# Optimization experiments

Measured on AMD Instinct MI355X. Metric: run time of the kernel, lower is better.

Reference implementation:

```python
import jax, jax.numpy as jnp
import numpy as np

IN_FEATURES = 1024
OUT_FEATURES = 1024
NUM_GRIDS = 8
GRID_MIN, GRID_MAX = -2.0, 2.0
DENOM = (GRID_MAX - GRID_MIN) / (NUM_GRIDS - 1)
LN_EPS = 1e-5
GRID = jnp.linspace(GRID_MIN, GRID_MAX, NUM_GRIDS)


def setup_inputs() -> dict:
    key = jax.random.key(0)
    k_x, k_sw, k_bw = jax.random.split(key, 3)
    N = 8192
    x = jax.random.normal(k_x, (N, IN_FEATURES), dtype=jnp.float32)
    ln_gamma = jnp.ones((IN_FEATURES,), dtype=jnp.float32)
    ln_beta = jnp.zeros((IN_FEATURES,), dtype=jnp.float32)
    # trunc_normal(std=0.1) approximated by scaled normal
    spline_w = 0.1 * jax.random.normal(k_sw, (OUT_FEATURES, IN_FEATURES * NUM_GRIDS), dtype=jnp.float32)
    base_w = jax.random.normal(k_bw, (OUT_FEATURES, IN_FEATURES), dtype=jnp.float32) * (1.0 / np.sqrt(IN_FEATURES))
    base_b = jnp.zeros((OUT_FEATURES,), dtype=jnp.float32)
    return {"x": x, "ln_gamma": ln_gamma, "ln_beta": ln_beta,
            "spline_w": spline_w, "base_w": base_w, "base_b": base_b}


def reference(x, ln_gamma, ln_beta, spline_w, base_w, base_b):
    # LayerNorm over last dim
    mu = jnp.mean(x, axis=-1, keepdims=True)
    var = jnp.var(x, axis=-1, keepdims=True)
    xn = (x - mu) * jax.lax.rsqrt(var + LN_EPS) * ln_gamma + ln_beta
    # RBF basis: [N, in, G]
    basis = jnp.exp(-jnp.square((xn[..., None] - GRID) / DENOM))
    basis = basis.reshape(x.shape[0], IN_FEATURES * NUM_GRIDS)
    y = jnp.einsum('nk,ok->no', basis, spline_w)
    y = y + jnp.einsum('nd,od->no', jax.nn.silu(x), base_w) + base_b
    return y
```

## Files before the change

### kernel.cpp

```cpp
#include <hip/hip_runtime.h>
#include <hip/hip_bf16.h>
#include <stdint.h>

#define IN_F 1024
#define OUT_F 1024
#define NG 8
#define KSPLINE 8192
#define KDIM 9216
#define KHALF 4608
#define M_ROWS 8192
#define LOG2E 1.4426950408889634f
#define KC 2.1019642153762872f

#define A_BLOCKS (M_ROWS / 4)
#define W_BLOCKS ((OUT_F * 2304) / 256)
#define RB (KDIM * 2)

using half4v = __attribute__((ext_vector_type(4))) _Float16;
using half8  = __attribute__((ext_vector_type(8))) _Float16;
using f32x4  = __attribute__((ext_vector_type(4))) float;

#define AS1 __attribute__((address_space(1)))
#define AS3 __attribute__((address_space(3)))

__global__ __launch_bounds__(256) void prep_kernel(
        const float* __restrict__ x, const float* __restrict__ gamma,
        const float* __restrict__ beta, const float* __restrict__ sw,
        const float* __restrict__ bw, _Float16* __restrict__ A,
        _Float16* __restrict__ W) {
    if (blockIdx.x >= A_BLOCKS) {
        int idx = (blockIdx.x - A_BLOCKS) * 256 + threadIdx.x;
        int o   = idx / 2304;
        int k4  = idx - o * 2304;
        float4 v;
        if (k4 < 2048) v = ((const float4*)sw)[(size_t)o * 2048 + k4];
        else           v = ((const float4*)bw)[(size_t)o * 256 + (k4 - 2048)];
        half4v h = { (_Float16)v.x, (_Float16)v.y, (_Float16)v.z, (_Float16)v.w };
        *(half4v*)(W + (size_t)idx * 4) = h;
        return;
    }
    const int wave = threadIdx.x >> 6, lane = threadIdx.x & 63;
    const int row = blockIdx.x * 4 + wave;
    const float* xr = x + (size_t)row * IN_F;

    float xv[16];
    float s = 0.0f, s2 = 0.0f;
#pragma unroll
    for (int j = 0; j < 16; ++j) {
        float v = xr[j * 64 + lane];
        xv[j] = v;
        s += v;
        s2 += v * v;
    }
#pragma unroll
    for (int off = 32; off > 0; off >>= 1) {
        s  += __shfl_xor(s, off);
        s2 += __shfl_xor(s2, off);
    }
    float mu   = s * (1.0f / IN_F);
    float var  = s2 * (1.0f / IN_F) - mu * mu;
    float rstd = rsqrtf(var + 1e-5f);

    const float cq[8] = {
        -2.0000000f * KC, -1.4285715f * KC, -0.8571429f * KC, -0.2857143f * KC,
         0.2857143f * KC,  0.8571429f * KC,  1.4285715f * KC,  2.0000000f * KC };

    _Float16* Arow = A + (size_t)row * KDIM;
    half8* basis_out = (half8*)Arow;
    _Float16* silu_out = Arow + KSPLINE;
#pragma unroll
    for (int j = 0; j < 16; ++j) {
        int f = j * 64 + lane;
        float xs = xv[j];
        float xq = ((xs - mu) * rstd * gamma[f] + beta[f]) * KC;
        half8 h;
#pragma unroll
        for (int g = 0; g < 8; ++g) {
            float v = xq - cq[g];
            h[g] = (_Float16)exp2f(-(v * v));
        }
        basis_out[f] = h;
        silu_out[f] = (_Float16)(xs / (1.0f + exp2f(-xs * LOG2E)));
    }
}

__global__ __launch_bounds__(512, 2) void gemm_kernel(
        const _Float16* __restrict__ A, const _Float16* __restrict__ W,
        const float* __restrict__ bias, float* __restrict__ C,
        float* __restrict__ P, int ntiles, int gpz) {
    extern __shared__ __align__(16) char smem[];
    const int tid  = threadIdx.x;
    const int wave = tid >> 6, lane = tid & 63;
    const int wm = wave >> 2, wn = wave & 3;

    const int lb = blockIdx.x;
    const int per_xcd = gridDim.x >> 5;
    const int xcd = lb & 7, sl = lb >> 3;
    const int g  = xcd * per_xcd + (sl >> 2);
    const int bn = sl & 3;
    const int bm = g / gpz;
    const int z  = g - bm * gpz;

    const int l8 = lane >> 3;
    const int chunkswz = ((lane & 7) ^ l8) << 4;
    const size_t zoff = (size_t)z * (KHALF * 2);
    const int gA[4] = {0, 128, 64, 192};
    const int gB[4] = {0, 128, 32, 160};
    const char* pA[4];
    const char* pB[4];
#pragma unroll
    for (int s = 0; s < 4; ++s) {
        pA[s] = (const char*)A + (size_t)(bm * 256 + gA[s] + wave * 8 + l8) * RB
                + zoff + chunkswz;
        pB[s] = (const char*)W + (size_t)(bn * 256 + gB[s] + (wave >> 2) * 64
                + (wave & 3) * 8 + l8) * RB + zoff + chunkswz;
    }

#define STAGE_A(s, nb, colb) __builtin_amdgcn_global_load_lds( \
        (const AS1 void*)(pA[s] + (colb)), \
        (AS3 void*)(smem + (nb) + (s) * 8192 + wave * 1024), 16, 0, 0)
#define STAGE_B(s, nb, colb) __builtin_amdgcn_global_load_lds( \
        (const AS1 void*)(pB[s] + (colb)), \
        (AS3 void*)(smem + (nb) + 32768 + (s) * 8192 + wave * 1024), 16, 0, 0)

    const int lm  = lane & 15;
    const int hi  = (lane >> 4) << 4;
    const int swz = (lm & 7) << 4;
    const int ck0 = (0  + hi) ^ swz;
    const int ck1 = (64 + hi) ^ swz;
    const int aB0 = (0 + wm) * 8192 + lm * 128;
    const int aB1 = (2 + wm) * 8192 + lm * 128;
    const int bB0 = 32768 + (0 + (wn >> 1)) * 8192 + ((wn & 1) * 32 + lm) * 128;
    const int bB1 = 32768 + (2 + (wn >> 1)) * 8192 + ((wn & 1) * 32 + lm) * 128;

    f32x4 acc[8][4] = {};

    STAGE_A(0, 0, 0); STAGE_A(1, 0, 0);
    STAGE_B(0, 0, 0); STAGE_B(1, 0, 0);
    STAGE_B(2, 0, 0); STAGE_B(3, 0, 0);
    STAGE_A(2, 0, 0); STAGE_A(3, 0, 0);
    asm volatile("s_waitcnt vmcnt(4)" ::: "memory");
    __builtin_amdgcn_s_barrier();

    for (int kt = 0; kt < ntiles; ++kt) {
        const int cb = (kt & 1) * 65536;
        const int nb = cb ^ 65536;
        const size_t col = (size_t)(kt + 1) * 128;
        const bool pref = (kt + 1 < ntiles);

        half8 aF[4][2], bF[2][2];
#pragma unroll
        for (int m = 0; m < 4; ++m) {
            aF[m][0] = *(const half8*)(smem + cb + aB0 + m * 2048 + ck0);
            aF[m][1] = *(const half8*)(smem + cb + aB0 + m * 2048 + ck1);
        }
#pragma unroll
        for (int n = 0; n < 2; ++n) {
            bF[n][0] = *(const half8*)(smem + cb + bB0 + n * 2048 + ck0);
            bF[n][1] = *(const half8*)(smem + cb + bB0 + n * 2048 + ck1);
        }
        asm volatile("s_waitcnt vmcnt(2)" ::: "memory");
        if (pref) { STAGE_A(0, nb, col); STAGE_A(1, nb, col); }
        asm volatile("s_waitcnt lgkmcnt(8)" ::: "memory");
        __builtin_amdgcn_s_barrier();
        asm volatile("s_waitcnt lgkmcnt(0)" ::: "memory");
        __builtin_amdgcn_s_setprio(1);
#pragma unroll
        for (int n = 0; n < 2; ++n)
#pragma unroll
            for (int m = 0; m < 4; ++m)
                acc[m][n] = __builtin_amdgcn_mfma_f32_16x16x32_f16(aF[m][0], bF[n][0], acc[m][n], 0, 0, 0);
#pragma unroll
        for (int n = 0; n < 2; ++n)
#pragma unroll
            for (int m = 0; m < 4; ++m)
                acc[m][n] = __builtin_amdgcn_mfma_f32_16x16x32_f16(aF[m][1], bF[n][1], acc[m][n], 0, 0, 0);
        __builtin_amdgcn_s_setprio(0);
        __builtin_amdgcn_s_barrier();

        half8 bG[2][2];
#pragma unroll
        for (int n = 0; n < 2; ++n) {
            bG[n][0] = *(const half8*)(smem + cb + bB1 + n * 2048 + ck0);
            bG[n][1] = *(const half8*)(smem + cb + bB1 + n * 2048 + ck1);
        }
        if (pref) {
            asm volatile("s_waitcnt vmcnt(2)" ::: "memory");
            STAGE_B(0, nb, col); STAGE_B(1, nb, col);
        } else {
            asm volatile("s_waitcnt vmcnt(0)" ::: "memory");
        }
        __builtin_amdgcn_s_barrier();
        asm volatile("s_waitcnt lgkmcnt(0)" ::: "memory");
        __builtin_amdgcn_s_setprio(1);
#pragma unroll
        for (int n = 0; n < 2; ++n)
#pragma unroll
            for (int m = 0; m < 4; ++m)
                acc[m][2 + n] = __builtin_amdgcn_mfma_f32_16x16x32_f16(aF[m][0], bG[n][0], acc[m][2 + n], 0, 0, 0);
#pragma unroll
        for (int n = 0; n < 2; ++n)
#pragma unroll
            for (int m = 0; m < 4; ++m)
                acc[m][2 + n] = __builtin_amdgcn_mfma_f32_16x16x32_f16(aF[m][1], bG[n][1], acc[m][2 + n], 0, 0, 0);
        __builtin_amdgcn_s_setprio(0);
        __builtin_amdgcn_s_barrier();

        half8 aG[4][2];
#pragma unroll
        for (int m = 0; m < 4; ++m) {
            aG[m][0] = *(const half8*)(smem + cb + aB1 + m * 2048 + ck0);
            aG[m][1] = *(const half8*)(smem + cb + aB1 + m * 2048 + ck1);
        }
        if (pref) { STAGE_B(2, nb, col); STAGE_B(3, nb, col); }
        __builtin_amdgcn_s_barrier();
        asm volatile("s_waitcnt lgkmcnt(0)" ::: "memory");
        __builtin_amdgcn_s_setprio(1);
#pragma unroll
        for (int n = 0; n < 2; ++n)
#pragma unroll
            for (int m = 0; m < 4; ++m)
                acc[4 + m][n] = __builtin_amdgcn_mfma_f32_16x16x32_f16(aG[m][0], bF[n][0], acc[4 + m][n], 0, 0, 0);
#pragma unroll
        for (int n = 0; n < 2; ++n)
#pragma unroll
            for (int m = 0; m < 4; ++m)
                acc[4 + m][n] = __builtin_amdgcn_mfma_f32_16x16x32_f16(aG[m][1], bF[n][1], acc[4 + m][n], 0, 0, 0);
        __builtin_amdgcn_s_setprio(0);
        __builtin_amdgcn_s_barrier();

        if (pref) {
            asm volatile("s_waitcnt vmcnt(2)" ::: "memory");
            STAGE_A(2, nb, col); STAGE_A(3, nb, col);
        }
        __builtin_amdgcn_s_barrier();
        __builtin_amdgcn_s_setprio(1);
#pragma unroll
        for (int n = 0; n < 2; ++n)
#pragma unroll
            for (int m = 0; m < 4; ++m)
                acc[4 + m][2 + n] = __builtin_amdgcn_mfma_f32_16x16x32_f16(aG[m][0], bG[n][0], acc[4 + m][2 + n], 0, 0, 0);
#pragma unroll
        for (int n = 0; n < 2; ++n)
#pragma unroll
            for (int m = 0; m < 4; ++m)
                acc[4 + m][2 + n] = __builtin_amdgcn_mfma_f32_16x16x32_f16(aG[m][1], bG[n][1], acc[4 + m][2 + n], 0, 0, 0);
        __builtin_amdgcn_s_setprio(0);
        __builtin_amdgcn_s_barrier();
    }

    const int cn  = lane & 15;
    const int rm4 = (lane >> 4) * 4;
    float* dst = z ? P : C;
#pragma unroll
    for (int nf = 0; nf < 4; ++nf) {
        int col = bn * 256 + wn * 64 + nf * 16 + cn;
        float bv = z ? 0.0f : bias[col];
#pragma unroll
        for (int mf = 0; mf < 8; ++mf) {
            int row = bm * 256 + wm * 128 + mf * 16 + rm4;
            float* cp = dst + (size_t)row * OUT_F + col;
#pragma unroll
            for (int r = 0; r < 4; ++r)
                cp[(size_t)r * OUT_F] = acc[mf][nf][r] + bv;
        }
    }
}

__global__ __launch_bounds__(256) void reduce_kernel(float* __restrict__ C,
        const float* __restrict__ P) {
    const int n4 = M_ROWS * OUT_F / 4;
    float4* c4 = (float4*)C;
    const float4* p4 = (const float4*)P;
    for (int i = blockIdx.x * 256 + threadIdx.x; i < n4; i += 2048 * 256) {
        float4 a = c4[i];
        float4 b = p4[i];
        a.x += b.x; a.y += b.y; a.z += b.z; a.w += b.w;
        c4[i] = a;
    }
}

extern "C" void kernel_launch(void* const* d_in, const int* in_sizes, int n_in,
                              void* d_out, int out_size, void* d_ws, size_t ws_size,
                              hipStream_t stream) {
    const float* x     = (const float*)d_in[0];
    const float* gamma = (const float*)d_in[1];
    const float* beta  = (const float*)d_in[2];
    const float* sw    = (const float*)d_in[3];
    const float* bw    = (const float*)d_in[4];
    const float* bb    = (const float*)d_in[5];
    float* out = (float*)d_out;

    char* ws = (char*)d_ws;
    size_t offW = 0;
    size_t offA = (size_t)OUT_F * KDIM * 2;
    size_t offP = offA + (size_t)M_ROWS * KDIM * 2;
    size_t need = offP + (size_t)M_ROWS * OUT_F * 4;
    _Float16* Wb = (_Float16*)(ws + offW);
    _Float16* Ab = (_Float16*)(ws + offA);
    float*    Pb = (float*)(ws + offP);
    const int split = (ws_size >= need);

    static int s_attr = 0;
    if (!s_attr) {
        hipFuncSetAttribute(reinterpret_cast<const void*>(gemm_kernel),
                            hipFuncAttributeMaxDynamicSharedMemorySize, 131072);
        s_attr = 1;
    }

    prep_kernel<<<A_BLOCKS + W_BLOCKS, 256, 0, stream>>>(
        x, gamma, beta, sw, bw, Ab, Wb);
    if (split) {
        gemm_kernel<<<256, 512, 131072, stream>>>(Ab, Wb, bb, out, Pb, KHALF / 64, 2);
        reduce_kernel<<<2048, 256, 0, stream>>>(out, Pb);
    } else {
        gemm_kernel<<<128, 512, 131072, stream>>>(Ab, Wb, bb, out, Pb, KDIM / 64, 1);
    }
}
```

Measured before the change: 287.8 us.

## Software-pipeline LDS fragment loads across K tiles with ping-pong register sets

Result: slower. 989.3 us (+243.7%).

```diff
diff --git a/kernel.cpp b/kernel.cpp
--- a/kernel.cpp
+++ b/kernel.cpp
@@ -134,119 +134,106 @@
     const int bB1 = 32768 + (2 + (wn >> 1)) * 8192 + ((wn & 1) * 32 + lm) * 128;
 
     f32x4 acc[8][4] = {};
+    half8 aE[4][2], bE[2][2], aO[4][2], bO[2][2];
+
+#define MFMA8(mb, Aa, Bb, nb2)                                                  \
+    {                                                                           \
+        _Pragma("unroll")                                                       \
+        for (int n = 0; n < 2; ++n)                                             \
+            _Pragma("unroll")                                                   \
+            for (int m = 0; m < 4; ++m)                                         \
+                acc[(mb)+m][(nb2)+n] = __builtin_amdgcn_mfma_f32_16x16x32_f16(  \
+                    Aa[m][0], Bb[n][0], acc[(mb)+m][(nb2)+n], 0, 0, 0);         \
+        _Pragma("unroll")                                                       \
+        for (int n = 0; n < 2; ++n)                                             \
+            _Pragma("unroll")                                                   \
+            for (int m = 0; m < 4; ++m)                                         \
+                acc[(mb)+m][(nb2)+n] = __builtin_amdgcn_mfma_f32_16x16x32_f16(  \
+                    Aa[m][1], Bb[n][1], acc[(mb)+m][(nb2)+n], 0, 0, 0);         \
+    }
+
+#define BAR_MFMA(mb, Aa, Bb, nb2)                                               \
+    __builtin_amdgcn_s_barrier();                                               \
+    asm volatile("s_waitcnt lgkmcnt(0)" ::: "memory");                          \
+    __builtin_amdgcn_sched_barrier(0);                                          \
+    __builtin_amdgcn_s_setprio(1);                                              \
+    MFMA8(mb, Aa, Bb, nb2)                                                      \
+    __builtin_amdgcn_s_setprio(0);                                              \
+    __builtin_amdgcn_s_barrier();
+
+#define TILE(cb, nb, AC, BC, AN, BN, colb, pref)                                \
+    {        \
+        half8 b1[2][2];                                                         \
+        _Pragma("unroll")                                                       \
+        for (int n = 0; n < 2; ++n) {                                           \
+            b1[n][0] = *(const half8*)(smem + (cb) + bB1 + n * 2048 + ck0);     \
+            b1[n][1] = *(const half8*)(smem + (cb) + bB1 + n * 2048 + ck1);     \
+        }                                                                       \
+        if (pref) { STAGE_A(0, nb, colb); STAGE_A(1, nb, colb);                 \
+            asm volatile("s_waitcnt vmcnt(2)" ::: "memory"); }                  \
+        else asm volatile("s_waitcnt vmcnt(0)" ::: "memory");                   \
+        BAR_MFMA(0, AC, BC, 0)                                                  \
+              \
+        half8 a1[4][2];                                                         \
+        _Pragma("unroll")                                                       \
+        for (int m = 0; m < 4; ++m) {                                           \
+            a1[m][0] = *(const half8*)(smem + (cb) + aB1 + m * 2048 + ck0);     \
+            a1[m][1] = *(const half8*)(smem + (cb) + aB1 + m * 2048 + ck1);     \
+        }                                                                       \
+        if (pref) { STAGE_B(0, nb, colb); STAGE_B(1, nb, colb);                 \
+            asm volatile("s_waitcnt vmcnt(2)" ::: "memory"); }                  \
+        else asm volatile("s_waitcnt vmcnt(0)" ::: "memory");                   \
+        BAR_MFMA(0, AC, b1, 2)                                                  \
+         \
+        if (pref) {                                                             \
+            _Pragma("unroll")                                                   \
+            for (int m = 0; m < 2; ++m) {                                       \
+                AN[m][0] = *(const half8*)(smem + (nb) + aB0 + m * 2048 + ck0); \
+                AN[m][1] = *(const half8*)(smem + (nb) + aB0 + m * 2048 + ck1); \
+            }                                                                   \
+            STAGE_B(2, nb, colb); STAGE_B(3, nb, colb);                         \
+            asm volatile("s_waitcnt vmcnt(2)" ::: "memory");                    \
+        }                                                                       \
+        BAR_MFMA(4, a1, BC, 0)                                                  \
+        \
+        \
+        if (pref) {                                                             \
+            _Pragma("unroll")                                                   \
+            for (int m = 2; m < 4; ++m) {                                       \
+                AN[m][0] = *(const half8*)(smem + (nb) + aB0 + m * 2048 + ck0); \
+                AN[m][1] = *(const half8*)(smem + (nb) + aB0 + m * 2048 + ck1); \
+            }                                                                   \
+            _Pragma("unroll")                                                   \
+            for (int n = 0; n < 2; ++n) {                                       \
+                BN[n][0] = *(const half8*)(smem + (nb) + bB0 + n * 2048 + ck0); \
+                BN[n][1] = *(const half8*)(smem + (nb) + bB0 + n * 2048 + ck1); \
+            }                                                                   \
+            STAGE_A(2, nb, colb); STAGE_A(3, nb, colb);                         \
+            asm volatile("s_waitcnt vmcnt(2)" ::: "memory");                    \
+        }                                                                       \
+        BAR_MFMA(4, a1, b1, 2)                                                  \
+    }
 
     STAGE_A(0, 0, 0); STAGE_A(1, 0, 0);
     STAGE_B(0, 0, 0); STAGE_B(1, 0, 0);
     STAGE_B(2, 0, 0); STAGE_B(3, 0, 0);
     STAGE_A(2, 0, 0); STAGE_A(3, 0, 0);
-    asm volatile("s_waitcnt vmcnt(4)" ::: "memory");
+    asm volatile("s_waitcnt vmcnt(2)" ::: "memory");
     __builtin_amdgcn_s_barrier();
-
-    for (int kt = 0; kt < ntiles; ++kt) {
-        const int cb = (kt & 1) * 65536;
-        const int nb = cb ^ 65536;
-        const size_t col = (size_t)(kt + 1) * 128;
-        const bool pref = (kt + 1 < ntiles);
-
-        half8 aF[4][2], bF[2][2];
-#pragma unroll
-        for (int m = 0; m < 4; ++m) {
-            aF[m][0] = *(const half8*)(smem + cb + aB0 + m * 2048 + ck0);
-            aF[m][1] = *(const half8*)(smem + cb + aB0 + m * 2048 + ck1);
-        }
-#pragma unroll
-        for (int n = 0; n < 2; ++n) {
-            bF[n][0] = *(const half8*)(smem + cb + bB0 + n * 2048 + ck0);
-            bF[n][1] = *(const half8*)(smem + cb + bB0 + n * 2048 + ck1);
-        }
-        asm volatile("s_waitcnt vmcnt(2)" ::: "memory");
-        if (pref) { STAGE_A(0, nb, col); STAGE_A(1, nb, col); }
-        asm volatile("s_waitcnt lgkmcnt(8)" ::: "memory");
-        __builtin_amdgcn_s_barrier();
-        asm volatile("s_waitcnt lgkmcnt(0)" ::: "memory");
-        __builtin_amdgcn_s_setprio(1);
-#pragma unroll
-        for (int n = 0; n < 2; ++n)
-#pragma unroll
-            for (int m = 0; m < 4; ++m)
-                acc[m][n] = __builtin_amdgcn_mfma_f32_16x16x32_f16(aF[m][0], bF[n][0], acc[m][n], 0, 0, 0);
-#pragma unroll
-        for (int n = 0; n < 2; ++n)
-#pragma unroll
-            for (int m = 0; m < 4; ++m)
-                acc[m][n] = __builtin_amdgcn_mfma_f32_16x16x32_f16(aF[m][1], bF[n][1], acc[m][n], 0, 0, 0);
-        __builtin_amdgcn_s_setprio(0);
-        __builtin_amdgcn_s_barrier();
-
-        half8 bG[2][2];
-#pragma unroll
-        for (int n = 0; n < 2; ++n) {
-            bG[n][0] = *(const half8*)(smem + cb + bB1 + n * 2048 + ck0);
-            bG[n][1] = *(const half8*)(smem + cb + bB1 + n * 2048 + ck1);
-        }
-        if (pref) {
-            asm volatile("s_waitcnt vmcnt(2)" ::: "memory");
-            STAGE_B(0, nb, col); STAGE_B(1, nb, col);
-        } else {
-            asm volatile("s_waitcnt vmcnt(0)" ::: "memory");
-        }
-        __builtin_amdgcn_s_barrier();
-        asm volatile("s_waitcnt lgkmcnt(0)" ::: "memory");
-        __builtin_amdgcn_s_setprio(1);
-#pragma unroll
-        for (int n = 0; n < 2; ++n)
-#pragma unroll
-            for (int m = 0; m < 4; ++m)
-                acc[m][2 + n] = __builtin_amdgcn_mfma_f32_16x16x32_f16(aF[m][0], bG[n][0], acc[m][2 + n], 0, 0, 0);
-#pragma unroll
-        for (int n = 0; n < 2; ++n)
-#pragma unroll
-            for (int m = 0; m < 4; ++m)
-                acc[m][2 + n] = __builtin_amdgcn_mfma_f32_16x16x32_f16(aF[m][1], bG[n][1], acc[m][2 + n], 0, 0, 0);
-        __builtin_amdgcn_s_setprio(0);
-        __builtin_amdgcn_s_barrier();
-
-        half8 aG[4][2];
-#pragma unroll
-        for (int m = 0; m < 4; ++m) {
-            aG[m][0] = *(const half8*)(smem + cb + aB1 + m * 2048 + ck0);
-            aG[m][1] = *(const half8*)(smem + cb + aB1 + m * 2048 + ck1);
-        }
-        if (pref) { STAGE_B(2, nb, col); STAGE_B(3, nb, col); }
-        __builtin_amdgcn_s_barrier();
-        asm volatile("s_waitcnt lgkmcnt(0)" ::: "memory");
-        __builtin_amdgcn_s_setprio(1);
-#pragma unroll
-        for (int n = 0; n < 2; ++n)
-#pragma unroll
-            for (int m = 0; m < 4; ++m)
-                acc[4 + m][n] = __builtin_amdgcn_mfma_f32_16x16x32_f16(aG[m][0], bF[n][0], acc[4 + m][n], 0, 0, 0);
-#pragma unroll
-        for (int n = 0; n < 2; ++n)
-#pragma unroll
-            for (int m = 0; m < 4; ++m)
-                acc[4 + m][n] = __builtin_amdgcn_mfma_f32_16x16x32_f16(aG[m][1], bF[n][1], acc[4 + m][n], 0, 0, 0);
-        __builtin_amdgcn_s_setprio(0);
-        __builtin_amdgcn_s_barrier();
-
-        if (pref) {
-            asm volatile("s_waitcnt vmcnt(2)" ::: "memory");
-            STAGE_A(2, nb, col); STAGE_A(3, nb, col);
-        }
-        __builtin_amdgcn_s_barrier();
-        __builtin_amdgcn_s_setprio(1);
-#pragma unroll
-        for (int n = 0; n < 2; ++n)
-#pragma unroll
-            for (int m = 0; m < 4; ++m)
-                acc[4 + m][2 + n] = __builtin_amdgcn_mfma_f32_16x16x32_f16(aG[m][0], bG[n][0], acc[4 + m][2 + n], 0, 0, 0);
-#pragma unroll
-        for (int n = 0; n < 2; ++n)
-#pragma unroll
-            for (int m = 0; m < 4; ++m)
-                acc[4 + m][2 + n] = __builtin_amdgcn_mfma_f32_16x16x32_f16(aG[m][1], bG[n][1], acc[4 + m][2 + n], 0, 0, 0);
-        __builtin_amdgcn_s_setprio(0);
-        __builtin_amdgcn_s_barrier();
+#pragma unroll
+    for (int m = 0; m < 4; ++m) {
+        aE[m][0] = *(const half8*)(smem + aB0 + m * 2048 + ck0);
+        aE[m][1] = *(const half8*)(smem + aB0 + m * 2048 + ck1);
+    }
+#pragma unroll
+    for (int n = 0; n < 2; ++n) {
+        bE[n][0] = *(const half8*)(smem + bB0 + n * 2048 + ck0);
+        bE[n][1] = *(const half8*)(smem + bB0 + n * 2048 + ck1);
+    }
+
+    for (int kt = 0; kt < ntiles; kt += 2) {
+        TILE(0, 65536, aE, bE, aO, bO, (size_t)(kt + 1) * 128, true)
+        TILE(65536, 0, aO, bO, aE, bE, (size_t)(kt + 2) * 128, (kt + 2 < ntiles))
     }
 
     const int cn  = lane & 15;
```
